# Performance work log

Measured on AMD Instinct MI355X. Metric: run time of the kernel, lower is better.

## Reference

```python
import jax, jax.numpy as jnp
import numpy as np

B, C, NH = 2, 128, 4
H = W = D = 28
WS = 7
SHIFT = 3
N = WS * WS * WS            # 343 tokens per window
HD = C // NH                # 32
SCALE = HD ** -0.5
HIDDEN = int(C * 4.0)
EPS = 1e-5


def _rel_pos_index():
    coords = np.stack(np.meshgrid(np.arange(WS), np.arange(WS), np.arange(WS), indexing='ij'))
    cf = coords.reshape(3, -1)                      # (3, N)
    rel = cf[:, :, None] - cf[:, None, :]           # (3, N, N)
    rel = rel.transpose(1, 2, 0) + (WS - 1)         # (N, N, 3), shifted to >=0
    idx = rel[..., 0] * (2 * WS - 1) ** 2 + rel[..., 1] * (2 * WS - 1) + rel[..., 2]
    return jnp.asarray(idx, dtype=jnp.int32)        # (N, N)


def setup_inputs() -> dict:
    key = jax.random.key(0)
    ks = jax.random.split(key, 16)
    s = 0.02
    return {
        'x': jax.random.normal(ks[0], (B, H * W * D, C), jnp.float32),
        'norm1_w': jnp.ones((C,), jnp.float32),
        'norm1_b': jnp.zeros((C,), jnp.float32),
        'qkv_w': jax.random.normal(ks[1], (3 * C, C), jnp.float32) * s,
        'qkv_b': jnp.zeros((3 * C,), jnp.float32),
        'rpb_table': jax.random.normal(ks[2], ((2 * WS - 1) ** 3, NH), jnp.float32) * s,
        'proj_w': jax.random.normal(ks[3], (C, C), jnp.float32) * s,
        'proj_b': jnp.zeros((C,), jnp.float32),
        'norm2_w': jnp.ones((C,), jnp.float32),
        'norm2_b': jnp.zeros((C,), jnp.float32),
        'mlp_w1': jax.random.normal(ks[4], (HIDDEN, C), jnp.float32) * s,
        'mlp_b1': jnp.zeros((HIDDEN,), jnp.float32),
        'mlp_w2': jax.random.normal(ks[5], (C, HIDDEN), jnp.float32) * s,
        'mlp_b2': jnp.zeros((C,), jnp.float32),
        'rel_idx': _rel_pos_index(),
    }


def _layernorm(x, w, b):
    mu = jnp.mean(x, axis=-1, keepdims=True)
    var = jnp.mean(jnp.square(x - mu), axis=-1, keepdims=True)
    return (x - mu) * jax.lax.rsqrt(var + EPS) * w + b


def _window_partition(x):
    # (B,H,W,D,C) -> (B*nW, N, C)
    x = x.reshape(B, H // WS, WS, W // WS, WS, D // WS, WS, C)
    x = x.transpose(0, 1, 3, 5, 2, 4, 6, 7)
    return x.reshape(-1, N, C)


def _window_reverse(wins):
    # (B*nW, N, C) -> (B,H,W,D,C)
    x = wins.reshape(B, H // WS, W // WS, D // WS, WS, WS, WS, C)
    x = x.transpose(0, 1, 4, 2, 5, 3, 6, 7)
    return x.reshape(B, H, W, D, C)


def _window_attention(xw, qkv_w, qkv_b, rpb_table, rel_idx, proj_w, proj_b):
    Bw = xw.shape[0]
    qkv = xw @ qkv_w.T + qkv_b                       # (Bw, N, 3C)
    qkv = qkv.reshape(Bw, N, 3, NH, HD).transpose(2, 0, 3, 1, 4)
    q, k, v = qkv[0], qkv[1], qkv[2]                 # each (Bw, NH, N, HD)
    attn = jnp.einsum('bhnd,bhmd->bhnm', q * SCALE, k)
    bias = rpb_table[rel_idx.reshape(-1)].reshape(N, N, NH).transpose(2, 0, 1)
    attn = jax.nn.softmax(attn + bias[None], axis=-1)
    out = jnp.einsum('bhnm,bhmd->bhnd', attn, v)     # (Bw, NH, N, HD)
    out = out.transpose(0, 2, 1, 3).reshape(Bw, N, C)
    return out @ proj_w.T + proj_b


def reference(x, norm1_w, norm1_b, qkv_w, qkv_b, rpb_table, proj_w, proj_b,
              norm2_w, norm2_b, mlp_w1, mlp_b1, mlp_w2, mlp_b2, rel_idx):
    shortcut = x
    h = _layernorm(x, norm1_w, norm1_b).reshape(B, H, W, D, C)
    if SHIFT > 0:
        h = jnp.roll(h, shift=(-SHIFT, -SHIFT, -SHIFT), axis=(1, 2, 3))
    wins = _window_partition(h)
    wins = _window_attention(wins, qkv_w, qkv_b, rpb_table, rel_idx, proj_w, proj_b)
    h = _window_reverse(wins)
    if SHIFT > 0:
        h = jnp.roll(h, shift=(SHIFT, SHIFT, SHIFT), axis=(1, 2, 3))
    x = shortcut + h.reshape(B, H * W * D, C)
    m = _layernorm(x, norm2_w, norm2_b)
    m = jax.nn.gelu(m @ mlp_w1.T + mlp_b1, approximate=False) @ mlp_w2.T + mlp_b2
    return x + m
```

## Files before the change

### kernel.cpp

```cpp
#include <hip/hip_runtime.h>

typedef __bf16 bfv8 __attribute__((ext_vector_type(8)));
typedef float f32x4 __attribute__((ext_vector_type(4)));
#define MFMA16(a,b,c) __builtin_amdgcn_mfma_f32_16x16x32_bf16(a,b,c,0,0,0)

constexpr int C      = 128;
constexpr int HD     = 32;
constexpr int NTOK   = 343;
constexpr int ROWS   = 43904;
constexpr int HIDDEN = 512;
constexpr float SCALE = 0.17677669529663687f;
constexpr float EPS   = 1e-5f;
constexpr int NT = 22;

static __device__ __forceinline__ float b2f(ushort u) {
  union { unsigned int i; float f; } x; x.i = ((unsigned int)u) << 16; return x.f;
}
static __device__ __forceinline__ ushort f2b(float f) {
  union { float f; unsigned int i; } x; x.f = f;
  unsigned int r = x.i + 0x7fffu + ((x.i >> 16) & 1u);
  return (ushort)(r >> 16);
}

static __device__ __forceinline__ int perm_row(int row) {
  int win = row / NTOK, tok = row - win * NTOK;
  int bb = win >> 6, wi = win & 63;
  int a  = wi >> 4, w2 = (wi >> 2) & 3, c2 = wi & 3;
  int t1 = tok / 49, rem = tok - t1 * 49;
  int t2 = rem / 7,  t3 = rem - t2 * 7;
  int gh = a * 7 + t1 + 3;  if (gh >= 28) gh -= 28;
  int gw = w2 * 7 + t2 + 3; if (gw >= 28) gw -= 28;
  int gd = c2 * 7 + t3 + 3; if (gd >= 28) gd -= 28;
  return bb * 21952 + gh * 784 + gw * 28 + gd;
}

__global__ __launch_bounds__(256) void cvt_kernel(const float* __restrict__ s0,
                                                  const float* __restrict__ s1,
                                                  const float* __restrict__ s2,
                                                  const float* __restrict__ s3,
                                                  ushort* __restrict__ d0,
                                                  ushort* __restrict__ d1,
                                                  ushort* __restrict__ d2,
                                                  ushort* __restrict__ d3) {
  int t = blockIdx.x * 256 + threadIdx.x;
  if (t < 49152)       d0[t]          = f2b(s0[t]);
  else if (t < 65536)  d1[t - 49152]  = f2b(s1[t - 49152]);
  else if (t < 131072) d2[t - 65536]  = f2b(s2[t - 65536]);
  else                 d3[t - 131072] = f2b(s3[t - 131072]);
}

__global__ __launch_bounds__(256) void bias_kernel(const int* __restrict__ rel,
                                                   const float* __restrict__ tab,
                                                   float4* __restrict__ biasr) {
  int t = blockIdx.x * 256 + threadIdx.x;
  if (t >= 4 * NT * NT * 64) return;
  int lane = t & 63;
  int nt   = (t >> 6) % NT;
  int mt   = ((t >> 6) / NT) % NT;
  int head = t / (64 * NT * NT);
  int k  = nt * 16 + (lane & 15);
  int qb = mt * 16 + (lane >> 4) * 4;
  float vv[4];
  #pragma unroll
  for (int r = 0; r < 4; ++r) {
    int q = qb + r;
    if (q < NTOK && k < NTOK) {
      int idx = rel[q * NTOK + k];
      vv[r] = tab[idx * 4 + head];
    } else {
      vv[r] = -3e38f;
    }
  }
  biasr[t] = make_float4(vv[0], vv[1], vv[2], vv[3]);
}

template<bool PERM>
__global__ __launch_bounds__(256) void ln_kernel(const float* __restrict__ in,
                                                 const float* __restrict__ w,
                                                 const float* __restrict__ b,
                                                 ushort* __restrict__ out) {
  int wid = threadIdx.x >> 6, lane = threadIdx.x & 63;
  int row = blockIdx.x * 4 + wid;
  int src = PERM ? perm_row(row) : row;
  float2 v = *reinterpret_cast<const float2*>(in + (size_t)src * C + lane * 2);
  float s = v.x + v.y, q = v.x * v.x + v.y * v.y;
  #pragma unroll
  for (int off = 32; off; off >>= 1) { s += __shfl_xor(s, off); q += __shfl_xor(q, off); }
  float mu = s * (1.0f / 128.0f);
  float var = q * (1.0f / 128.0f) - mu * mu;
  float rs = rsqrtf(var + EPS);
  int c = lane * 2;
  ushort2 ov;
  ov.x = f2b((v.x - mu) * rs * w[c]     + b[c]);
  ov.y = f2b((v.y - mu) * rs * w[c + 1] + b[c + 1]);
  *reinterpret_cast<ushort2*>(out + (size_t)row * C + c) = ov;
}

template<int KTOT, int EPI>
__global__ __launch_bounds__(256) void gemm_kernel(const ushort* __restrict__ A,
                                                   const ushort* __restrict__ W,
                                                   const float* __restrict__ bias,
                                                   const float* __restrict__ X,
                                                   ushort* __restrict__ O0,
                                                   ushort* __restrict__ O1,
                                                   ushort* __restrict__ O2,
                                                   float* __restrict__ OF) {
  __shared__ ushort Al[128][136];
  __shared__ ushort Bl[128][136];
  const int m0 = blockIdx.y * 128, n0 = blockIdx.x * 128;
  const int tid = threadIdx.x, lane = tid & 63, wid = tid >> 6;
  const int wr = wid >> 1, wc = wid & 1;
  const int lr = lane & 15, kb0 = (lane >> 4) * 8;
  const int sr = tid >> 4, sc = (tid & 15) * 8;
  f32x4 acc[4][4] = {};
  for (int kc = 0; kc < KTOT; kc += 128) {
    #pragma unroll
    for (int p = 0; p < 8; ++p) {
      int row = p * 16 + sr;
      *reinterpret_cast<int4*>(&Al[row][sc]) =
          *reinterpret_cast<const int4*>(&A[(size_t)(m0 + row) * KTOT + kc + sc]);
      *reinterpret_cast<int4*>(&Bl[row][sc]) =
          *reinterpret_cast<const int4*>(&W[(size_t)(n0 + row) * KTOT + kc + sc]);
    }
    __syncthreads();
    #pragma unroll
    for (int kk = 0; kk < 4; ++kk) {
      int kb = kk * 32 + kb0;
      bfv8 a[4], b[4];
      #pragma unroll
      for (int m = 0; m < 4; ++m) a[m] = *reinterpret_cast<const bfv8*>(&Al[wr * 64 + m * 16 + lr][kb]);
      #pragma unroll
      for (int n = 0; n < 4; ++n) b[n] = *reinterpret_cast<const bfv8*>(&Bl[wc * 64 + n * 16 + lr][kb]);
      #pragma unroll
      for (int m = 0; m < 4; ++m)
        #pragma unroll
        for (int n = 0; n < 4; ++n)
          acc[m][n] = MFMA16(a[m], b[n], acc[m][n]);
    }
    __syncthreads();
  }
  #pragma unroll
  for (int m = 0; m < 4; ++m)
    #pragma unroll
    for (int n = 0; n < 4; ++n)
      #pragma unroll
      for (int r = 0; r < 4; ++r) {
        int gm = m0 + wr * 64 + m * 16 + (lane >> 4) * 4 + r;
        int gn = n0 + wc * 64 + n * 16 + (lane & 15);
        float v = acc[m][n][r] + bias[gn];
        if (EPI == 0) {
          int which = gn >> 7, head = (gn >> 5) & 3, d = gn & 31;
          if (which == 0) v *= SCALE;
          int win = gm / NTOK, tok = gm - win * NTOK;
          ushort* dst = (which == 0) ? O0 : (which == 1) ? O1 : O2;
          dst[((win * 4 + head) * NTOK + tok) * HD + d] = f2b(v);
        } else {
          int orig = perm_row(gm);
          OF[(size_t)orig * C + gn] = v + X[(size_t)orig * C + gn];
        }
      }
}

__global__ __launch_bounds__(256) void mlp_kernel(const float* __restrict__ y,
                                                  const float* __restrict__ nw,
                                                  const float* __restrict__ nb,
                                                  const ushort* __restrict__ W1,
                                                  const float* __restrict__ b1,
                                                  const ushort* __restrict__ W2,
                                                  const float* __restrict__ b2,
                                                  float* __restrict__ outp) {
  __shared__ ushort AH[64][140];
  __shared__ ushort Wb1[64][140];
  __shared__ ushort Wb2[128][70];
  const int m0 = blockIdx.x * 64;
  const int tid = threadIdx.x, lane = tid & 63, wave = tid >> 6;
  const int sr = tid >> 4, sc = (tid & 15) * 8;
  int4 wpre[4];
  #pragma unroll
  for (int p = 0; p < 4; ++p)
    wpre[p] = *reinterpret_cast<const int4*>(&W1[(size_t)(p * 16 + sr) * 128 + sc]);
  {
    int row = tid >> 2, sub = tid & 3;
    const float* yr = y + (size_t)(m0 + row) * C + sub * 32;
    float4 v[8];
    float s = 0.f, q = 0.f;
    #pragma unroll
    for (int j = 0; j < 8; ++j) {
      v[j] = *reinterpret_cast<const float4*>(yr + j * 4);
      s += v[j].x + v[j].y + v[j].z + v[j].w;
      q += v[j].x * v[j].x + v[j].y * v[j].y + v[j].z * v[j].z + v[j].w * v[j].w;
    }
    s += __shfl_xor(s, 1); q += __shfl_xor(q, 1);
    s += __shfl_xor(s, 2); q += __shfl_xor(q, 2);
    float mu = s * (1.0f / 128.0f);
    float var = q * (1.0f / 128.0f) - mu * mu;
    float rs = rsqrtf(var + EPS);
    #pragma unroll
    for (int j = 0; j < 8; ++j) {
      int c = sub * 32 + j * 4;
      ushort4 o;
      o.x = f2b((v[j].x - mu) * rs * nw[c]     + nb[c]);
      o.y = f2b((v[j].y - mu) * rs * nw[c + 1] + nb[c + 1]);
      o.z = f2b((v[j].z - mu) * rs * nw[c + 2] + nb[c + 2]);
      o.w = f2b((v[j].w - mu) * rs * nw[c + 3] + nb[c + 3]);
      *reinterpret_cast<ushort4*>(&AH[row][c]) = o;
    }
  }
  const int lr = lane & 15, kb0 = (lane >> 4) * 8;
  const int key = lane & 15, qr4 = (lane >> 4) * 4;
  bfv8 af[4];
  #pragma unroll
  for (int kk = 0; kk < 4; ++kk)
    af[kk] = *reinterpret_cast<const bfv8*>(&AH[wave * 16 + lr][kk * 32 + kb0]);
  #pragma unroll
  for (int p = 0; p < 4; ++p)
    *reinterpret_cast<int4*>(&Wb1[p * 16 + sr][sc]) = wpre[p];
  __syncthreads();
  #pragma unroll
  for (int p = 0; p < 4; ++p) {
    int idx = p * 256 + tid;
    wpre[p] = *reinterpret_cast<const int4*>(&W2[(size_t)(idx >> 3) * HIDDEN + (idx & 7) * 8]);
  }
  f32x4 acc[8] = {};
  for (int c = 0; c < 8; ++c) {
    #pragma unroll
    for (int n = 0; n < 4; ++n) {
      f32x4 h = {};
      #pragma unroll
      for (int kk = 0; kk < 4; ++kk)
        h = MFMA16(af[kk], *reinterpret_cast<const bfv8*>(&Wb1[n * 16 + lr][kk * 32 + kb0]), h);
      #pragma unroll
      for (int r = 0; r < 4; ++r) {
        float val = h[r] + b1[c * 64 + n * 16 + key];
        float g = 0.5f * val * (1.0f + erff(val * 0.70710678118654752f));
        AH[wave * 16 + qr4 + r][n * 16 + key] = f2b(g);
      }
    }
    bfv8 hf[2];
    #pragma unroll
    for (int kk = 0; kk < 2; ++kk)
      hf[kk] = *reinterpret_cast<const bfv8*>(&AH[wave * 16 + lr][kk * 32 + kb0]);
    #pragma unroll
    for (int p = 0; p < 4; ++p) {
      int idx = p * 256 + tid;
      *reinterpret_cast<int4*>(&Wb2[idx >> 3][(idx & 7) * 8]) = wpre[p];
    }
    __syncthreads();
    if (c < 7) {
      #pragma unroll
      for (int p = 0; p < 4; ++p)
        wpre[p] = *reinterpret_cast<const int4*>(&W1[(size_t)((c + 1) * 64 + p * 16 + sr) * 128 + sc]);
    }
    #pragma unroll
    for (int n = 0; n < 8; ++n)
      #pragma unroll
      for (int kk = 0; kk < 2; ++kk)
        acc[n] = MFMA16(hf[kk], *reinterpret_cast<const bfv8*>(&Wb2[n * 16 + lr][kk * 32 + kb0]), acc[n]);
    if (c < 7) {
      #pragma unroll
      for (int p = 0; p < 4; ++p)
        *reinterpret_cast<int4*>(&Wb1[p * 16 + sr][sc]) = wpre[p];
      __syncthreads();
      #pragma unroll
      for (int p = 0; p < 4; ++p) {
        int idx = p * 256 + tid;
        wpre[p] = *reinterpret_cast<const int4*>(&W2[(size_t)(idx >> 3) * HIDDEN + (c + 1) * 64 + (idx & 7) * 8]);
      }
    }
  }
  #pragma unroll
  for (int n = 0; n < 8; ++n)
    #pragma unroll
    for (int r = 0; r < 4; ++r) {
      int gm = m0 + wave * 16 + qr4 + r;
      int gn = n * 16 + key;
      outp[(size_t)gm * C + gn] = acc[n][r] + b2[gn] + y[(size_t)gm * C + gn];
    }
}

__global__ __launch_bounds__(512) void attn_kernel(const ushort* __restrict__ Q,
                                                   const ushort* __restrict__ K,
                                                   const ushort* __restrict__ V,
                                                   const f32x4* __restrict__ biasr,
                                                   ushort* __restrict__ out) {
  __shared__ ushort vt[32][360];
  __shared__ ushort pl[8][16][204];
  const int wh = blockIdx.x;
  const int win = wh >> 2, head = wh & 3;
  const int tid = threadIdx.x, lane = tid & 63, wave = tid >> 6;
  if (tid < 352) {
    int t = tid;
    if (t < NTOK) {
      ushort tmp[32];
      const ushort* vr = V + ((size_t)wh * NTOK + t) * HD;
      *reinterpret_cast<int4*>(&tmp[0])  = *reinterpret_cast<const int4*>(vr);
      *reinterpret_cast<int4*>(&tmp[8])  = *reinterpret_cast<const int4*>(vr + 8);
      *reinterpret_cast<int4*>(&tmp[16]) = *reinterpret_cast<const int4*>(vr + 16);
      *reinterpret_cast<int4*>(&tmp[24]) = *reinterpret_cast<const int4*>(vr + 24);
      #pragma unroll
      for (int d = 0; d < 32; ++d) vt[d][t] = tmp[d];
    } else {
      #pragma unroll
      for (int d = 0; d < 32; ++d) vt[d][t] = 0;
    }
  }
  __syncthreads();
  const int lr = lane & 15, kb0 = (lane >> 4) * 8;
  const int key = lane & 15, qr4 = (lane >> 4) * 4;
  for (int mt = wave; mt < NT; mt += 8) {
    int qrow = mt * 16 + lr; if (qrow > 342) qrow = 342;
    bfv8 aq = *reinterpret_cast<const bfv8*>(Q + ((size_t)wh * NTOK + qrow) * HD + kb0);
    const f32x4* bR = biasr + ((size_t)(head * NT + mt) * NT) * 64 + lane;
    float sm[4] = {0.f, 0.f, 0.f, 0.f};
    f32x4 o0 = {}, o1 = {};
    #pragma unroll
    for (int nt = 0; nt < 12; ++nt) {
      int krow = nt * 16 + lr;
      bfv8 bk = *reinterpret_cast<const bfv8*>(K + ((size_t)wh * NTOK + krow) * HD + kb0);
      f32x4 s = MFMA16(aq, bk, bR[nt * 64]);
      int kcol = nt * 16 + key;
      #pragma unroll
      for (int r = 0; r < 4; ++r) {
        float p = __expf(s[r]);
        sm[r] += p;
        pl[wave][qr4 + r][kcol] = f2b(p);
      }
    }
    #pragma unroll
    for (int kt = 0; kt < 6; ++kt) {
      bfv8 bp  = *reinterpret_cast<const bfv8*>(&pl[wave][lr][kt * 32 + kb0]);
      bfv8 av0 = *reinterpret_cast<const bfv8*>(&vt[lr][kt * 32 + kb0]);
      bfv8 av1 = *reinterpret_cast<const bfv8*>(&vt[16 + lr][kt * 32 + kb0]);
      o0 = MFMA16(av0, bp, o0);
      o1 = MFMA16(av1, bp, o1);
    }
    #pragma unroll
    for (int nt = 12; nt < NT; ++nt) {
      int krow = nt * 16 + lr; if (krow > 342) krow = 342;
      bfv8 bk = *reinterpret_cast<const bfv8*>(K + ((size_t)wh * NTOK + krow) * HD + kb0);
      f32x4 s = MFMA16(aq, bk, bR[nt * 64]);
      int kcol = (nt - 12) * 16 + key;
      #pragma unroll
      for (int r = 0; r < 4; ++r) {
        float p = __expf(s[r]);
        sm[r] += p;
        pl[wave][qr4 + r][kcol] = f2b(p);
      }
    }
    #pragma unroll
    for (int kt = 0; kt < 5; ++kt) {
      bfv8 bp  = *reinterpret_cast<const bfv8*>(&pl[wave][lr][kt * 32 + kb0]);
      bfv8 av0 = *reinterpret_cast<const bfv8*>(&vt[lr][192 + kt * 32 + kb0]);
      bfv8 av1 = *reinterpret_cast<const bfv8*>(&vt[16 + lr][192 + kt * 32 + kb0]);
      o0 = MFMA16(av0, bp, o0);
      o1 = MFMA16(av1, bp, o1);
    }
    #pragma unroll
    for (int r = 0; r < 4; ++r) {
      #pragma unroll
      for (int off = 1; off < 16; off <<= 1) sm[r] += __shfl_xor(sm[r], off);
    }
    float inv[4];
    #pragma unroll
    for (int r = 0; r < 4; ++r) inv[r] = 1.0f / sm[r];
    int qcol = lane & 15;
    int srcl = (qcol >> 2) << 4;
    float i0 = __shfl(inv[0], srcl), i1 = __shfl(inv[1], srcl);
    float i2 = __shfl(inv[2], srcl), i3 = __shfl(inv[3], srcl);
    float invq = (qcol & 2) ? ((qcol & 1) ? i3 : i2) : ((qcol & 1) ? i1 : i0);
    int q = mt * 16 + qcol;
    if (q < NTOK) {
      int dbase = qr4;
      ushort4 r0, r1;
      r0.x = f2b(o0[0] * invq); r0.y = f2b(o0[1] * invq);
      r0.z = f2b(o0[2] * invq); r0.w = f2b(o0[3] * invq);
      r1.x = f2b(o1[0] * invq); r1.y = f2b(o1[1] * invq);
      r1.z = f2b(o1[2] * invq); r1.w = f2b(o1[3] * invq);
      ushort* ob = out + (size_t)(win * NTOK + q) * C + head * HD;
      *reinterpret_cast<ushort4*>(ob + dbase)      = r0;
      *reinterpret_cast<ushort4*>(ob + 16 + dbase) = r1;
    }
  }
}

extern "C" void kernel_launch(void* const* d_in, const int* in_sizes, int n_in,
                              void* d_out, int out_size, void* d_ws, size_t ws_size,
                              hipStream_t stream) {
  const float* x     = (const float*)d_in[0];
  const float* n1w   = (const float*)d_in[1];
  const float* n1b   = (const float*)d_in[2];
  const float* qkvw  = (const float*)d_in[3];
  const float* qkvb  = (const float*)d_in[4];
  const float* rpb   = (const float*)d_in[5];
  const float* projw = (const float*)d_in[6];
  const float* projb = (const float*)d_in[7];
  const float* n2w   = (const float*)d_in[8];
  const float* n2b   = (const float*)d_in[9];
  const float* w1    = (const float*)d_in[10];
  const float* b1    = (const float*)d_in[11];
  const float* w2    = (const float*)d_in[12];
  const float* b2    = (const float*)d_in[13];
  const int*   rel   = (const int*)d_in[14];

  char* ws = (char*)d_ws;
  constexpr size_t SZ_ACT  = (size_t)ROWS * C * 2;
  constexpr size_t SZ_BIAS = (size_t)4 * NT * NT * 64 * 16;

  ushort* lnbuf  = (ushort*)(ws);
  ushort* Qb     = (ushort*)(ws + SZ_ACT);
  ushort* Kb     = (ushort*)(ws + 2 * SZ_ACT);
  ushort* Vb     = (ushort*)(ws + 3 * SZ_ACT);
  f32x4*  biasr  = (f32x4*)(ws + 4 * SZ_ACT);
  size_t off_att = (4 * SZ_ACT + SZ_BIAS + 255) & ~(size_t)255;
  ushort* attout = (ushort*)(ws + off_att);
  size_t off_y   = off_att + SZ_ACT;
  float*  y      = (float*)(ws + off_y);
  size_t off_w   = off_y + (size_t)ROWS * C * 4;
  ushort* wqkv   = (ushort*)(ws + off_w);
  ushort* wproj  = (ushort*)(ws + off_w + 98304);
  ushort* wm1    = (ushort*)(ws + off_w + 131072);
  ushort* wm2    = (ushort*)(ws + off_w + 262144);
  float*  outp   = (float*)d_out;

  cvt_kernel<<<768, 256, 0, stream>>>(qkvw, projw, w1, w2, wqkv, wproj, wm1, wm2);
  bias_kernel<<<(4 * NT * NT * 64 + 255) / 256, 256, 0, stream>>>(rel, rpb, (float4*)biasr);
  ln_kernel<true><<<ROWS / 4, 256, 0, stream>>>(x, n1w, n1b, lnbuf);
  gemm_kernel<128, 0><<<dim3(3, 343), 256, 0, stream>>>(lnbuf, wqkv, qkvb, nullptr, Qb, Kb, Vb, nullptr);
  attn_kernel<<<512, 512, 0, stream>>>(Qb, Kb, Vb, biasr, attout);
  gemm_kernel<128, 1><<<dim3(1, 343), 256, 0, stream>>>(attout, wproj, projb, x, nullptr, nullptr, nullptr, y);
  mlp_kernel<<<ROWS / 64, 256, 0, stream>>>(y, n2w, n2b, wm1, b1, wm2, b2, outp);
}
```

Before: 147.0 us.

## Fold log2e into scale and bias for exp2 softmax; simplify MLP weight staging

The attention softmax now uses exp2f, with log2(e) folded into the Q scale and the relative-position bias table so that no per-element multiply is needed before the exponential. Separately, the MLP kernel drops its register-prefetch double buffering of the W1/W2 chunks. It now loads each chunk straight from global memory into LDS between two barriers at the start of every iteration, and pads the W2 tile row to 72. This removes register pressure and the extra sync points, but exposes global load latency that was previously overlapped with compute.

Result: no change. 147.0 us (-0.0%).

```diff
diff --git a/kernel.cpp b/kernel.cpp
--- a/kernel.cpp
+++ b/kernel.cpp
@@ -9,7 +9,8 @@
 constexpr int NTOK   = 343;
 constexpr int ROWS   = 43904;
 constexpr int HIDDEN = 512;
-constexpr float SCALE = 0.17677669529663687f;
+constexpr float SCALE_L2E = 0.25503486f;
+constexpr float LOG2E = 1.4426950408889634f;
 constexpr float EPS   = 1e-5f;
 constexpr int NT = 22;
 
@@ -66,9 +67,9 @@
     int q = qb + r;
     if (q < NTOK && k < NTOK) {
       int idx = rel[q * NTOK + k];
-      vv[r] = tab[idx * 4 + head];
+      vv[r] = tab[idx * 4 + head] * LOG2E;
     } else {
-      vv[r] = -3e38f;
+      vv[r] = -2e38f;
     }
   }
   biasr[t] = make_float4(vv[0], vv[1], vv[2], vv[3]);
@@ -150,7 +151,7 @@
         float v = acc[m][n][r] + bias[gn];
         if (EPI == 0) {
           int which = gn >> 7, head = (gn >> 5) & 3, d = gn & 31;
-          if (which == 0) v *= SCALE;
+          if (which == 0) v *= SCALE_L2E;
           int win = gm / NTOK, tok = gm - win * NTOK;
           ushort* dst = (which == 0) ? O0 : (which == 1) ? O1 : O2;
           dst[((win * 4 + head) * NTOK + tok) * HD + d] = f2b(v);
@@ -170,15 +171,11 @@
                                                   const float* __restrict__ b2,
                                                   float* __restrict__ outp) {
   __shared__ ushort AH[64][140];
-  __shared__ ushort Wb1[64][140];
-  __shared__ ushort Wb2[128][70];
+  __shared__ ushort Wl1[64][140];
+  __shared__ ushort Wl2[128][72];
   const int m0 = blockIdx.x * 64;
   const int tid = threadIdx.x, lane = tid & 63, wave = tid >> 6;
   const int sr = tid >> 4, sc = (tid & 15) * 8;
-  int4 wpre[4];
-  #pragma unroll
-  for (int p = 0; p < 4; ++p)
-    wpre[p] = *reinterpret_cast<const int4*>(&W1[(size_t)(p * 16 + sr) * 128 + sc]);
   {
     int row = tid >> 2, sub = tid & 3;
     const float* yr = y + (size_t)(m0 + row) * C + sub * 32;
@@ -212,23 +209,26 @@
   #pragma unroll
   for (int kk = 0; kk < 4; ++kk)
     af[kk] = *reinterpret_cast<const bfv8*>(&AH[wave * 16 + lr][kk * 32 + kb0]);
-  #pragma unroll
-  for (int p = 0; p < 4; ++p)
-    *reinterpret_cast<int4*>(&Wb1[p * 16 + sr][sc]) = wpre[p];
-  __syncthreads();
-  #pragma unroll
-  for (int p = 0; p < 4; ++p) {
-    int idx = p * 256 + tid;
-    wpre[p] = *reinterpret_cast<const int4*>(&W2[(size_t)(idx >> 3) * HIDDEN + (idx & 7) * 8]);
-  }
   f32x4 acc[8] = {};
   for (int c = 0; c < 8; ++c) {
+    __syncthreads();
+    #pragma unroll
+    for (int p = 0; p < 4; ++p)
+      *reinterpret_cast<int4*>(&Wl1[p * 16 + sr][sc]) =
+          *reinterpret_cast<const int4*>(&W1[(size_t)(c * 64 + p * 16 + sr) * 128 + sc]);
+    #pragma unroll
+    for (int p = 0; p < 4; ++p) {
+      int idx = p * 256 + tid;
+      *reinterpret_cast<int4*>(&Wl2[idx >> 3][(idx & 7) * 8]) =
+          *reinterpret_cast<const int4*>(&W2[(size_t)(idx >> 3) * HIDDEN + c * 64 + (idx & 7) * 8]);
+    }
+    __syncthreads();
     #pragma unroll
     for (int n = 0; n < 4; ++n) {
       f32x4 h = {};
       #pragma unroll
       for (int kk = 0; kk < 4; ++kk)
-        h = MFMA16(af[kk], *reinterpret_cast<const bfv8*>(&Wb1[n * 16 + lr][kk * 32 + kb0]), h);
+        h = MFMA16(af[kk], *reinterpret_cast<const bfv8*>(&Wl1[n * 16 + lr][kk * 32 + kb0]), h);
       #pragma unroll
       for (int r = 0; r < 4; ++r) {
         float val = h[r] + b1[c * 64 + n * 16 + key];
@@ -241,32 +241,10 @@
     for (int kk = 0; kk < 2; ++kk)
       hf[kk] = *reinterpret_cast<const bfv8*>(&AH[wave * 16 + lr][kk * 32 + kb0]);
     #pragma unroll
-    for (int p = 0; p < 4; ++p) {
-      int idx = p * 256 + tid;
-      *reinterpret_cast<int4*>(&Wb2[idx >> 3][(idx & 7) * 8]) = wpre[p];
-    }
-    __syncthreads();
-    if (c < 7) {
-      #pragma unroll
-      for (int p = 0; p < 4; ++p)
-        wpre[p] = *reinterpret_cast<const int4*>(&W1[(size_t)((c + 1) * 64 + p * 16 + sr) * 128 + sc]);
-    }
-    #pragma unroll
     for (int n = 0; n < 8; ++n)
       #pragma unroll
       for (int kk = 0; kk < 2; ++kk)
-        acc[n] = MFMA16(hf[kk], *reinterpret_cast<const bfv8*>(&Wb2[n * 16 + lr][kk * 32 + kb0]), acc[n]);
-    if (c < 7) {
-      #pragma unroll
-      for (int p = 0; p < 4; ++p)
-        *reinterpret_cast<int4*>(&Wb1[p * 16 + sr][sc]) = wpre[p];
-      __syncthreads();
-      #pragma unroll
-      for (int p = 0; p < 4; ++p) {
-        int idx = p * 256 + tid;
-        wpre[p] = *reinterpret_cast<const int4*>(&W2[(size_t)(idx >> 3) * HIDDEN + (c + 1) * 64 + (idx & 7) * 8]);
-      }
-    }
+        acc[n] = MFMA16(hf[kk], *reinterpret_cast<const bfv8*>(&Wl2[n * 16 + lr][kk * 32 + kb0]), acc[n]);
   }
   #pragma unroll
   for (int n = 0; n < 8; ++n)
@@ -321,7 +299,7 @@
       int kcol = nt * 16 + key;
       #pragma unroll
       for (int r = 0; r < 4; ++r) {
-        float p = __expf(s[r]);
+        float p = exp2f(s[r]);
         sm[r] += p;
         pl[wave][qr4 + r][kcol] = f2b(p);
       }
@@ -342,7 +320,7 @@
       int kcol = (nt - 12) * 16 + key;
       #pragma unroll
       for (int r = 0; r < 4; ++r) {
-        float p = __expf(s[r]);
+        float p = exp2f(s[r]);
         sm[r] += p;
         pl[wave][qr4 + r][kcol] = f2b(p);
       }
```
